# Performance work log

Hardware: AMD Instinct MI355X
Metric: run time of the kernel (lower is better)

The kernel has to match this reference:

```python
import jax, jax.numpy as jnp
import numpy as np

# Module hyperparameters (from init_kwargs / config defaults)
LOCAL_WINDOW = 128
GLOBAL_BUDGET = 64
ATT_BUDGET = 0.05
RANDOM_BUDGET = 0.1

B, S, D = 4, 4096, 1024


def setup_inputs() -> dict:
    key = jax.random.key(0)
    k1, k2 = jax.random.split(key)
    return {
        "hidden_states": jax.random.normal(k1, (B, S, D), dtype=jnp.float32),
        "attention_mask": jnp.ones((B, S), dtype=jnp.int32),
        "W_imp": jax.random.normal(k2, (1, D), dtype=jnp.float32) * 0.02,
    }


def _build_sparse_mask(hidden_states, attention_mask, W_imp):
    b, s, d = hidden_states.shape
    valid = attention_mask.astype(bool)                       # [b, s]
    # base mask: valid x valid, with causal constraint (is_decoder=True)
    i = jnp.arange(s)[:, None]
    j = jnp.arange(s)[None, :]
    causal = j <= i                                            # [s, s]
    base = (valid[:, None, :] & valid[:, :, None]) & causal[None]

    # 1) local causal sliding window: query i attends keys in [i-W+1, i]
    diff = i - j
    local = (diff >= 0) & (diff < LOCAL_WINDOW)                # [s, s]
    sparse = jnp.broadcast_to(local[None], (b, s, s))
    selected = jnp.broadcast_to(local.any(axis=0)[None], (b, s))

    # 2) global tokens via importance projection + top-k
    base_budget = min(GLOBAL_BUDGET, max(1, int(s * ATT_BUDGET)))
    scores = jnp.einsum('bsd,d->bs', hidden_states, W_imp[0])  # [b, s]
    scores = jnp.where(valid, scores, -jnp.inf)
    _, top_idx = jax.lax.top_k(scores, base_budget)            # [b, k]
    global_tokens = jnp.zeros((b, s), bool).at[
        jnp.arange(b)[:, None], top_idx].set(True)             # [b, s]
    # globals attend to everything and are attended by everything
    sparse = sparse | global_tokens[:, None, :] | global_tokens[:, :, None]
    selected = selected | global_tokens

    # 3) structured random tokens: deterministic strided selection
    r_budget = min(s, max(1, int(s * RANDOM_BUDGET)))
    stride = max(1, s // r_budget)
    rand_idx = (jnp.arange(r_budget) * stride) % s
    random_1d = jnp.zeros((s,), bool).at[rand_idx].set(True)
    random_tokens = jnp.broadcast_to(random_1d[None], (b, s))  # [b, s]
    sparse = sparse | random_tokens[:, None, :] | random_tokens[:, :, None]
    selected = selected | random_tokens

    # re-apply validity + causality
    sparse = sparse & base
    return sparse, selected, global_tokens, random_tokens


def reference(hidden_states, attention_mask, W_imp):
    b, s, _ = hidden_states.shape
    sparse, selected, gtok, rtok = _build_sparse_mask(
        hidden_states, attention_mask, W_imp)
    total_connections = sparse.sum(axis=(1, 2))
    attention_efficiency = total_connections.astype(jnp.float32) / float(s * s)
    # return sparse mask as float (the form consumed by attention), plus stats
    return (sparse.astype(jnp.float32), selected, attention_efficiency)
```

## Files before the change

### kernel.cpp

```cpp
#include <hip/hip_runtime.h>
#include <math.h>

#define BATCH 4
#define SEQ   4096
#define DIM   1024
#define TOPK  64
#define RSTRIDE 10
#define RBUDGET 409
#define LOCALW  128

typedef float nfloat4 __attribute__((ext_vector_type(4)));

#define WS_SCORES_OFF 0
#define WS_FLAGS_OFF  (BATCH * SEQ * sizeof(float))

__global__ void scores_kernel(const float* __restrict__ hs,
                              const int* __restrict__ amask,
                              const float* __restrict__ W,
                              float* __restrict__ scores) {
    int row  = blockIdx.x * 4 + (threadIdx.x >> 6);
    int lane = threadIdx.x & 63;
    const float4* h4 = (const float4*)(hs + (size_t)row * DIM);
    const float4* w4 = (const float4*)W;
    float acc = 0.0f;
#pragma unroll
    for (int k = 0; k < DIM / 4 / 64; ++k) {
        float4 h = h4[lane + 64 * k];
        float4 w = w4[lane + 64 * k];
        acc += h.x * w.x + h.y * w.y + h.z * w.z + h.w * w.w;
    }
#pragma unroll
    for (int off = 32; off; off >>= 1) acc += __shfl_down(acc, off, 64);
    if (lane == 0)
        scores[row] = amask[row] ? acc : -INFINITY;
}

__global__ void topk_flags_kernel(const float* __restrict__ scores,
                                  const int* __restrict__ amask,
                                  unsigned char* __restrict__ flags) {
    __shared__ unsigned int su[SEQ];
    __shared__ unsigned char gsel[SEQ];
    __shared__ unsigned int hist[257];
    __shared__ unsigned int sufA[257];
    __shared__ unsigned int sufB[257];
    __shared__ unsigned int bcast[2];

    int b = blockIdx.x, t = threadIdx.x;

    for (int k = t; k < SEQ; k += 256) {
        float s = scores[b * SEQ + k];
        unsigned int x = __float_as_uint(s);
        su[k] = (x & 0x80000000u) ? ~x : (x | 0x80000000u);
        gsel[k] = 0;
    }
    __syncthreads();

    unsigned int prefixVal = 0;
    unsigned int remaining = TOPK;
#pragma unroll
    for (int pass = 0; pass < 4; ++pass) {
        int shift = 24 - 8 * pass;
        unsigned int highmask = (pass == 0) ? 0u : (0xFFFFFFFFu << (shift + 8));

        hist[t] = 0;
        if (t == 0) hist[256] = 0;
        __syncthreads();

#pragma unroll
        for (int e = 0; e < SEQ / 256; ++e) {
            unsigned int u = su[t * (SEQ / 256) + e];
            if ((u & highmask) == prefixVal)
                atomicAdd(&hist[(u >> shift) & 0xFFu], 1u);
        }
        __syncthreads();

        sufA[t] = hist[t];
        if (t == 0) sufA[256] = 0;
        __syncthreads();
        unsigned int* src = sufA;
        unsigned int* dst = sufB;
        for (int d = 1; d < 256; d <<= 1) {
            unsigned int v = src[t] + ((t + d < 256) ? src[t + d] : 0u);
            dst[t] = v;
            if (t == 0) dst[256] = 0;
            __syncthreads();
            unsigned int* tmp = src; src = dst; dst = tmp;
        }
        if (src[t] >= remaining && src[t + 1] < remaining) {
            bcast[0] = (unsigned int)t;
            bcast[1] = remaining - src[t + 1];
        }
        __syncthreads();
        prefixVal |= (bcast[0] << shift);
        remaining = bcast[1];
        __syncthreads();
    }

    unsigned int T = prefixVal;
    unsigned int myeq = 0;
#pragma unroll
    for (int e = 0; e < SEQ / 256; ++e)
        if (su[t * (SEQ / 256) + e] == T) myeq++;
    sufA[t] = myeq;
    __syncthreads();
    {
        unsigned int* src = sufA;
        unsigned int* dst = sufB;
        for (int d = 1; d < 256; d <<= 1) {
            unsigned int v = src[t] + ((t >= d) ? src[t - d] : 0u);
            dst[t] = v;
            __syncthreads();
            unsigned int* tmp = src; src = dst; dst = tmp;
        }
        unsigned int taken = src[t] - myeq;
#pragma unroll
        for (int e = 0; e < SEQ / 256; ++e) {
            int idx = t * (SEQ / 256) + e;
            unsigned int u = su[idx];
            if (u > T) gsel[idx] = 1;
            else if (u == T) { if (taken < remaining) gsel[idx] = 1; taken++; }
        }
    }
    __syncthreads();

    for (int k = t; k < SEQ; k += 256) {
        int valid = (amask[b * SEQ + k] != 0) ? 1 : 0;
        int g = gsel[k];
        int r = ((k % RSTRIDE) == 0 && (k / RSTRIDE) < RBUDGET) ? 1 : 0;
        flags[b * SEQ + k] = (unsigned char)(valid | (g << 1) | (r << 2));
    }
}

__global__ void counts_kernel(const unsigned char* __restrict__ flags,
                              float* __restrict__ out_eff) {
    __shared__ int cumV[SEQ];
    __shared__ int cumH[SEQ];
    __shared__ int tvA[256], tvB[256], thA[256], thB[256];
    __shared__ int red[256];
    int b = blockIdx.x, t = threadIdx.x;
    int base = b * SEQ;

    int lv[16], lh[16];
    int sv = 0, sh = 0;
#pragma unroll
    for (int e = 0; e < 16; ++e) {
        unsigned char f = flags[base + t * 16 + e];
        int v = f & 1;
        int h = v & (((f & 6) != 0) ? 1 : 0);
        sv += v; sh += h;
        lv[e] = sv; lh[e] = sh;
    }
    tvA[t] = sv; thA[t] = sh;
    __syncthreads();
    int* vsrc = tvA; int* vdst = tvB;
    int* hsrc = thA; int* hdst = thB;
    for (int d = 1; d < 256; d <<= 1) {
        int av = vsrc[t] + ((t >= d) ? vsrc[t - d] : 0);
        int ah = hsrc[t] + ((t >= d) ? hsrc[t - d] : 0);
        vdst[t] = av; hdst[t] = ah;
        __syncthreads();
        int* tmp = vsrc; vsrc = vdst; vdst = tmp;
        tmp = hsrc; hsrc = hdst; hdst = tmp;
    }
    int bv = vsrc[t] - sv, bh = hsrc[t] - sh;
#pragma unroll
    for (int e = 0; e < 16; ++e) {
        cumV[t * 16 + e] = lv[e] + bv;
        cumH[t * 16 + e] = lh[e] + bh;
    }
    __syncthreads();

    int cnt = 0;
#pragma unroll
    for (int e = 0; e < 16; ++e) {
        int i = t * 16 + e;
        unsigned char f = flags[base + i];
        int validI = f & 1;
        int hotI = (f & 6) != 0;
        int c;
        if (hotI) c = cumV[i];
        else {
            int w = (i >= LOCALW) ? (cumV[i] - cumV[i - LOCALW]) : cumV[i];
            int g = (i >= LOCALW) ? cumH[i - LOCALW] : 0;
            c = w + g;
        }
        cnt += validI ? c : 0;
    }
    red[t] = cnt;
    __syncthreads();
    for (int s2 = 128; s2; s2 >>= 1) {
        if (t < s2) red[t] += red[t + s2];
        __syncthreads();
    }
    if (t == 0)
        out_eff[b] = (float)red[0] * (1.0f / ((float)SEQ * (float)SEQ));
}

__global__ void __launch_bounds__(256) mask_kernel(
        const unsigned char* __restrict__ flags,
        float* __restrict__ out) {
    int row0 = blockIdx.x << 2;
    int b = row0 >> 12;
    int t = threadIdx.x;

    const uchar4* f4 = (const uchar4*)(flags + b * SEQ);
    unsigned int validBits = 0, hotBits = 0;
#pragma unroll
    for (int k = 0; k < 4; ++k) {
        uchar4 f = f4[t + 256 * k];
        unsigned char fa[4] = {f.x, f.y, f.z, f.w};
#pragma unroll
        for (int e = 0; e < 4; ++e) {
            int idx = k * 4 + e;
            validBits |= (unsigned int)(fa[e] & 1u) << idx;
            hotBits   |= (unsigned int)((fa[e] & 6u) ? 1u : 0u) << idx;
        }
    }

    uchar4 fr = *(const uchar4*)(flags + row0);
    unsigned char fra[4] = {fr.x, fr.y, fr.z, fr.w};

#pragma unroll
    for (int r = 0; r < 4; ++r) {
        int i = (row0 + r) & (SEQ - 1);
        int validI = fra[r] & 1;
        int hotI = (fra[r] & 6) != 0;
        nfloat4* outrow4 = (nfloat4*)(out + (size_t)(row0 + r) * SEQ);
#pragma unroll
        for (int k = 0; k < 4; ++k) {
            int j4 = t + 256 * k;
            int j0 = j4 << 2;
            nfloat4 v;
#pragma unroll
            for (int e = 0; e < 4; ++e) {
                int idx = k * 4 + e;
                int j = j0 + e;
                int one = (j <= i) & validI & (int)((validBits >> idx) & 1u)
                        & (((i - j) < LOCALW) | hotI | (int)((hotBits >> idx) & 1u));
                v[e] = one ? 1.0f : 0.0f;
            }
            __builtin_nontemporal_store(v, outrow4 + j4);
        }
    }
}

__global__ void finalize_kernel(float* __restrict__ out_selected) {
    int idx = blockIdx.x * 256 + threadIdx.x;
    if (idx < BATCH * SEQ) out_selected[idx] = 1.0f;
}

extern "C" void kernel_launch(void* const* d_in, const int* in_sizes, int n_in,
                              void* d_out, int out_size, void* d_ws, size_t ws_size,
                              hipStream_t stream) {
    const float* hs    = (const float*)d_in[0];
    const int*   amask = (const int*)d_in[1];
    const float* W     = (const float*)d_in[2];

    char* ws = (char*)d_ws;
    float*         scores = (float*)(ws + WS_SCORES_OFF);
    unsigned char* flags  = (unsigned char*)(ws + WS_FLAGS_OFF);

    float* out_sparse   = (float*)d_out;
    float* out_selected = out_sparse + (size_t)BATCH * SEQ * SEQ;
    float* out_eff      = out_selected + BATCH * SEQ;

    scores_kernel<<<BATCH * SEQ / 4, 256, 0, stream>>>(hs, amask, W, scores);
    topk_flags_kernel<<<BATCH, 256, 0, stream>>>(scores, amask, flags);
    counts_kernel<<<BATCH, 256, 0, stream>>>(flags, out_eff);
    mask_kernel<<<BATCH * SEQ / 4, 256, 0, stream>>>(flags, out_sparse);
    finalize_kernel<<<(BATCH * SEQ + 255) / 256, 256, 0, stream>>>(out_selected);
}
```

Measured before the change: 336.3 us.

## Split mask writes into flag-independent and flag-dependent kernels, fuse topk/counts/finalize

The output mask is split into two regions. The part that depends only on the attention mask (causal window and the upper triangle) is written in the same launch as the top-k selection and the selected-ones fill. A second launch writes only the left region that depends on the global and random flags, and also computes the counts using bitmask popcounts instead of shared cumulative arrays. This cuts the launch count from five to three and overlaps the single-block top-k with the bulk store traffic. In exchange, the logic depends on the fixed window and column-boundary arithmetic, and the two kernels write disjoint pieces of the same output.

```diff
diff --git a/kernel.cpp b/kernel.cpp
--- a/kernel.cpp
+++ b/kernel.cpp
@@ -13,6 +13,11 @@
 
 #define WS_SCORES_OFF 0
 #define WS_FLAGS_OFF  (BATCH * SEQ * sizeof(float))
+
+#define X_TOPK_BLOCKS 4
+#define X_SEL_BLOCKS  16
+#define X_STATIC_BASE (X_TOPK_BLOCKS + X_SEL_BLOCKS)
+#define Y_CNT_BLOCKS  4
 
 __global__ void scores_kernel(const float* __restrict__ hs,
                               const int* __restrict__ amask,
@@ -35,9 +40,12 @@
         scores[row] = amask[row] ? acc : -INFINITY;
 }
 
-__global__ void topk_flags_kernel(const float* __restrict__ scores,
-                                  const int* __restrict__ amask,
-                                  unsigned char* __restrict__ flags) {
+__global__ void __launch_bounds__(256) fused_static_kernel(
+        const float* __restrict__ scores,
+        const int* __restrict__ amask,
+        unsigned char* __restrict__ flags,
+        float* __restrict__ out_sparse,
+        float* __restrict__ out_selected) {
     __shared__ unsigned int su[SEQ];
     __shared__ unsigned char gsel[SEQ];
     __shared__ unsigned int hist[257];
@@ -45,163 +53,219 @@
     __shared__ unsigned int sufB[257];
     __shared__ unsigned int bcast[2];
 
-    int b = blockIdx.x, t = threadIdx.x;
-
-    for (int k = t; k < SEQ; k += 256) {
-        float s = scores[b * SEQ + k];
-        unsigned int x = __float_as_uint(s);
-        su[k] = (x & 0x80000000u) ? ~x : (x | 0x80000000u);
-        gsel[k] = 0;
-    }
-    __syncthreads();
-
-    unsigned int prefixVal = 0;
-    unsigned int remaining = TOPK;
-#pragma unroll
-    for (int pass = 0; pass < 4; ++pass) {
-        int shift = 24 - 8 * pass;
-        unsigned int highmask = (pass == 0) ? 0u : (0xFFFFFFFFu << (shift + 8));
-
-        hist[t] = 0;
-        if (t == 0) hist[256] = 0;
-        __syncthreads();
-
-#pragma unroll
-        for (int e = 0; e < SEQ / 256; ++e) {
-            unsigned int u = su[t * (SEQ / 256) + e];
-            if ((u & highmask) == prefixVal)
-                atomicAdd(&hist[(u >> shift) & 0xFFu], 1u);
-        }
-        __syncthreads();
-
-        sufA[t] = hist[t];
-        if (t == 0) sufA[256] = 0;
-        __syncthreads();
-        unsigned int* src = sufA;
-        unsigned int* dst = sufB;
+    int bid = blockIdx.x;
+    int t = threadIdx.x;
+
+    if (bid < X_TOPK_BLOCKS) {
+        int b = bid;
+
+        for (int k = t; k < SEQ; k += 256) {
+            float s = scores[b * SEQ + k];
+            unsigned int x = __float_as_uint(s);
+            su[k] = (x & 0x80000000u) ? ~x : (x | 0x80000000u);
+            gsel[k] = 0;
+        }
+        __syncthreads();
+
+        unsigned int prefixVal = 0;
+        unsigned int remaining = TOPK;
+#pragma unroll
+        for (int pass = 0; pass < 4; ++pass) {
+            int shift = 24 - 8 * pass;
+            unsigned int highmask = (pass == 0) ? 0u : (0xFFFFFFFFu << (shift + 8));
+
+            hist[t] = 0;
+            if (t == 0) hist[256] = 0;
+            __syncthreads();
+
+#pragma unroll
+            for (int e = 0; e < SEQ / 256; ++e) {
+                unsigned int u = su[t * (SEQ / 256) + e];
+                if ((u & highmask) == prefixVal)
+                    atomicAdd(&hist[(u >> shift) & 0xFFu], 1u);
+            }
+            __syncthreads();
+
+            sufA[t] = hist[t];
+            if (t == 0) sufA[256] = 0;
+            __syncthreads();
+            unsigned int* src = sufA;
+            unsigned int* dst = sufB;
+            for (int d = 1; d < 256; d <<= 1) {
+                unsigned int v = src[t] + ((t + d < 256) ? src[t + d] : 0u);
+                dst[t] = v;
+                if (t == 0) dst[256] = 0;
+                __syncthreads();
+                unsigned int* tmp = src; src = dst; dst = tmp;
+            }
+            if (src[t] >= remaining && src[t + 1] < remaining) {
+                bcast[0] = (unsigned int)t;
+                bcast[1] = remaining - src[t + 1];
+            }
+            __syncthreads();
+            prefixVal |= (bcast[0] << shift);
+            remaining = bcast[1];
+            __syncthreads();
+        }
+
+        unsigned int T = prefixVal;
+        unsigned int myeq = 0;
+#pragma unroll
+        for (int e = 0; e < SEQ / 256; ++e)
+            if (su[t * (SEQ / 256) + e] == T) myeq++;
+        sufA[t] = myeq;
+        __syncthreads();
+        {
+            unsigned int* src = sufA;
+            unsigned int* dst = sufB;
+            for (int d = 1; d < 256; d <<= 1) {
+                unsigned int v = src[t] + ((t >= d) ? src[t - d] : 0u);
+                dst[t] = v;
+                __syncthreads();
+                unsigned int* tmp = src; src = dst; dst = tmp;
+            }
+            unsigned int taken = src[t] - myeq;
+#pragma unroll
+            for (int e = 0; e < SEQ / 256; ++e) {
+                int idx = t * (SEQ / 256) + e;
+                unsigned int u = su[idx];
+                if (u > T) gsel[idx] = 1;
+                else if (u == T) { if (taken < remaining) gsel[idx] = 1; taken++; }
+            }
+        }
+        __syncthreads();
+
+        for (int k = t; k < SEQ; k += 256) {
+            int valid = (amask[b * SEQ + k] != 0) ? 1 : 0;
+            int g = gsel[k];
+            int r = ((k % RSTRIDE) == 0 && (k / RSTRIDE) < RBUDGET) ? 1 : 0;
+            flags[b * SEQ + k] = (unsigned char)(valid | (g << 1) | (r << 2));
+        }
+        return;
+    }
+
+    if (bid < X_STATIC_BASE) {
+        int idx = (bid - X_TOPK_BLOCKS) * 256 + t;
+        nfloat4 ones = {1.0f, 1.0f, 1.0f, 1.0f};
+        __builtin_nontemporal_store(ones, ((nfloat4*)out_selected) + idx);
+        return;
+    }
+
+    int row0 = (bid - X_STATIC_BASE) << 2;
+    int b = row0 >> 12;
+
+    const int4* am4 = (const int4*)(amask + b * SEQ);
+    unsigned int validBits = 0;
+#pragma unroll
+    for (int k = 0; k < 4; ++k) {
+        int4 m = am4[t + 256 * k];
+        validBits |= (unsigned int)(m.x != 0) << (k * 4 + 0);
+        validBits |= (unsigned int)(m.y != 0) << (k * 4 + 1);
+        validBits |= (unsigned int)(m.z != 0) << (k * 4 + 2);
+        validBits |= (unsigned int)(m.w != 0) << (k * 4 + 3);
+    }
+    int4 mr = *(const int4*)(amask + row0);
+    int vIr[4] = {mr.x != 0, mr.y != 0, mr.z != 0, mr.w != 0};
+
+#pragma unroll
+    for (int r = 0; r < 4; ++r) {
+        int i = (row0 + r) & (SEQ - 1);
+        int vI = vIr[r];
+        int c4 = (i <= 127) ? 0 : (((i - 127 + 15) & ~15) >> 2);
+        nfloat4* outrow4 = (nfloat4*)(out_sparse + (size_t)(row0 + r) * SEQ);
+#pragma unroll
+        for (int k = 0; k < 4; ++k) {
+            int j4 = t + 256 * k;
+            if (j4 < c4) continue;
+            int j0 = j4 << 2;
+            nfloat4 v;
+#pragma unroll
+            for (int e = 0; e < 4; ++e) {
+                int j = j0 + e;
+                int one = (j <= i) & vI & (int)((validBits >> (k * 4 + e)) & 1u);
+                v[e] = one ? 1.0f : 0.0f;
+            }
+            __builtin_nontemporal_store(v, outrow4 + j4);
+        }
+    }
+}
+
+__global__ void __launch_bounds__(256) fused_dynamic_kernel(
+        const unsigned char* __restrict__ flags,
+        float* __restrict__ out_sparse,
+        float* __restrict__ out_eff) {
+    __shared__ unsigned int vb[256], hb[256];
+    __shared__ int tA[256], tB[256], tC[256], tD[256];
+    __shared__ int exV[256], exH[256];
+    __shared__ int red[256];
+
+    int bid = blockIdx.x, t = threadIdx.x;
+
+    if (bid < Y_CNT_BLOCKS) {
+        int b = bid, base = b * SEQ;
+        const unsigned char* fp = flags + base + t * 16;
+        unsigned int myv = 0, myh = 0;
+#pragma unroll
+        for (int e = 0; e < 16; ++e) {
+            unsigned char f = fp[e];
+            unsigned int v = f & 1u;
+            unsigned int h = v & ((f & 6u) ? 1u : 0u);
+            myv |= v << e;
+            myh |= h << e;
+        }
+        vb[t] = myv; hb[t] = myh;
+        int sv = __popc(myv), sh = __popc(myh);
+        tA[t] = sv; tC[t] = sh;
+        __syncthreads();
+        int* vsrc = tA; int* vdst = tB;
+        int* hsrc = tC; int* hdst = tD;
         for (int d = 1; d < 256; d <<= 1) {
-            unsigned int v = src[t] + ((t + d < 256) ? src[t + d] : 0u);
-            dst[t] = v;
-            if (t == 0) dst[256] = 0;
-            __syncthreads();
-            unsigned int* tmp = src; src = dst; dst = tmp;
-        }
-        if (src[t] >= remaining && src[t + 1] < remaining) {
-            bcast[0] = (unsigned int)t;
-            bcast[1] = remaining - src[t + 1];
-        }
-        __syncthreads();
-        prefixVal |= (bcast[0] << shift);
-        remaining = bcast[1];
-        __syncthreads();
-    }
-
-    unsigned int T = prefixVal;
-    unsigned int myeq = 0;
-#pragma unroll
-    for (int e = 0; e < SEQ / 256; ++e)
-        if (su[t * (SEQ / 256) + e] == T) myeq++;
-    sufA[t] = myeq;
-    __syncthreads();
-    {
-        unsigned int* src = sufA;
-        unsigned int* dst = sufB;
-        for (int d = 1; d < 256; d <<= 1) {
-            unsigned int v = src[t] + ((t >= d) ? src[t - d] : 0u);
-            dst[t] = v;
-            __syncthreads();
-            unsigned int* tmp = src; src = dst; dst = tmp;
-        }
-        unsigned int taken = src[t] - myeq;
-#pragma unroll
-        for (int e = 0; e < SEQ / 256; ++e) {
-            int idx = t * (SEQ / 256) + e;
-            unsigned int u = su[idx];
-            if (u > T) gsel[idx] = 1;
-            else if (u == T) { if (taken < remaining) gsel[idx] = 1; taken++; }
-        }
-    }
-    __syncthreads();
-
-    for (int k = t; k < SEQ; k += 256) {
-        int valid = (amask[b * SEQ + k] != 0) ? 1 : 0;
-        int g = gsel[k];
-        int r = ((k % RSTRIDE) == 0 && (k / RSTRIDE) < RBUDGET) ? 1 : 0;
-        flags[b * SEQ + k] = (unsigned char)(valid | (g << 1) | (r << 2));
-    }
-}
-
-__global__ void counts_kernel(const unsigned char* __restrict__ flags,
-                              float* __restrict__ out_eff) {
-    __shared__ int cumV[SEQ];
-    __shared__ int cumH[SEQ];
-    __shared__ int tvA[256], tvB[256], thA[256], thB[256];
-    __shared__ int red[256];
-    int b = blockIdx.x, t = threadIdx.x;
-    int base = b * SEQ;
-
-    int lv[16], lh[16];
-    int sv = 0, sh = 0;
-#pragma unroll
-    for (int e = 0; e < 16; ++e) {
-        unsigned char f = flags[base + t * 16 + e];
-        int v = f & 1;
-        int h = v & (((f & 6) != 0) ? 1 : 0);
-        sv += v; sh += h;
-        lv[e] = sv; lh[e] = sh;
-    }
-    tvA[t] = sv; thA[t] = sh;
-    __syncthreads();
-    int* vsrc = tvA; int* vdst = tvB;
-    int* hsrc = thA; int* hdst = thB;
-    for (int d = 1; d < 256; d <<= 1) {
-        int av = vsrc[t] + ((t >= d) ? vsrc[t - d] : 0);
-        int ah = hsrc[t] + ((t >= d) ? hsrc[t - d] : 0);
-        vdst[t] = av; hdst[t] = ah;
-        __syncthreads();
-        int* tmp = vsrc; vsrc = vdst; vdst = tmp;
-        tmp = hsrc; hsrc = hdst; hdst = tmp;
-    }
-    int bv = vsrc[t] - sv, bh = hsrc[t] - sh;
-#pragma unroll
-    for (int e = 0; e < 16; ++e) {
-        cumV[t * 16 + e] = lv[e] + bv;
-        cumH[t * 16 + e] = lh[e] + bh;
-    }
-    __syncthreads();
-
-    int cnt = 0;
-#pragma unroll
-    for (int e = 0; e < 16; ++e) {
-        int i = t * 16 + e;
-        unsigned char f = flags[base + i];
-        int validI = f & 1;
-        int hotI = (f & 6) != 0;
-        int c;
-        if (hotI) c = cumV[i];
-        else {
-            int w = (i >= LOCALW) ? (cumV[i] - cumV[i - LOCALW]) : cumV[i];
-            int g = (i >= LOCALW) ? cumH[i - LOCALW] : 0;
-            c = w + g;
-        }
-        cnt += validI ? c : 0;
-    }
-    red[t] = cnt;
-    __syncthreads();
-    for (int s2 = 128; s2; s2 >>= 1) {
-        if (t < s2) red[t] += red[t + s2];
-        __syncthreads();
-    }
-    if (t == 0)
-        out_eff[b] = (float)red[0] * (1.0f / ((float)SEQ * (float)SEQ));
-}
-
-__global__ void __launch_bounds__(256) mask_kernel(
-        const unsigned char* __restrict__ flags,
-        float* __restrict__ out) {
-    int row0 = blockIdx.x << 2;
+            int av = vsrc[t] + ((t >= d) ? vsrc[t - d] : 0);
+            int ah = hsrc[t] + ((t >= d) ? hsrc[t - d] : 0);
+            vdst[t] = av; hdst[t] = ah;
+            __syncthreads();
+            int* tmp = vsrc; vsrc = vdst; vdst = tmp;
+            tmp = hsrc; hsrc = hdst; hdst = tmp;
+        }
+        exV[t] = vsrc[t] - sv;
+        exH[t] = hsrc[t] - sh;
+        __syncthreads();
+
+        int exVt = exV[t];
+        int exV8 = (t >= 8) ? exV[t - 8] : 0;
+        int exH8 = (t >= 8) ? exH[t - 8] : 0;
+        unsigned int vb8 = (t >= 8) ? vb[t - 8] : 0u;
+        unsigned int hb8 = (t >= 8) ? hb[t - 8] : 0u;
+        int cnt = 0;
+#pragma unroll
+        for (int e = 0; e < 16; ++e) {
+            unsigned int m = (2u << e) - 1u;
+            int validI = (int)((myv >> e) & 1u);
+            int hotI   = (int)((myh >> e) & 1u);
+            int cumVi = exVt + __popc(myv & m);
+            int c;
+            if (t >= 8) {
+                int cumVm = exV8 + __popc(vb8 & m);
+                int cumHm = exH8 + __popc(hb8 & m);
+                c = hotI ? cumVi : (cumVi - cumVm + cumHm);
+            } else {
+                c = cumVi;
+            }
+            cnt += validI ? c : 0;
+        }
+        red[t] = cnt;
+        __syncthreads();
+        for (int s2 = 128; s2; s2 >>= 1) {
+            if (t < s2) red[t] += red[t + s2];
+            __syncthreads();
+        }
+        if (t == 0)
+            out_eff[b] = (float)red[0] * (1.0f / ((float)SEQ * (float)SEQ));
+        return;
+    }
+
+    int row0 = (bid - Y_CNT_BLOCKS) << 2;
     int b = row0 >> 12;
-    int t = threadIdx.x;
 
     const uchar4* f4 = (const uchar4*)(flags + b * SEQ);
     unsigned int validBits = 0, hotBits = 0;
@@ -216,37 +280,34 @@
             hotBits   |= (unsigned int)((fa[e] & 6u) ? 1u : 0u) << idx;
         }
     }
-
     uchar4 fr = *(const uchar4*)(flags + row0);
     unsigned char fra[4] = {fr.x, fr.y, fr.z, fr.w};
 
 #pragma unroll
     for (int r = 0; r < 4; ++r) {
         int i = (row0 + r) & (SEQ - 1);
-        int validI = fra[r] & 1;
+        if (i <= 127) continue;
+        int vI = fra[r] & 1;
         int hotI = (fra[r] & 6) != 0;
-        nfloat4* outrow4 = (nfloat4*)(out + (size_t)(row0 + r) * SEQ);
+        int c4 = ((i - 127 + 15) & ~15) >> 2;
+        nfloat4* outrow4 = (nfloat4*)(out_sparse + (size_t)(row0 + r) * SEQ);
 #pragma unroll
         for (int k = 0; k < 4; ++k) {
             int j4 = t + 256 * k;
+            if (j4 >= c4) continue;
             int j0 = j4 << 2;
             nfloat4 v;
 #pragma unroll
             for (int e = 0; e < 4; ++e) {
                 int idx = k * 4 + e;
                 int j = j0 + e;
-                int one = (j <= i) & validI & (int)((validBits >> idx) & 1u)
+                int one = vI & (int)((validBits >> idx) & 1u)
                         & (((i - j) < LOCALW) | hotI | (int)((hotBits >> idx) & 1u));
                 v[e] = one ? 1.0f : 0.0f;
             }
             __builtin_nontemporal_store(v, outrow4 + j4);
         }
     }
-}
-
-__global__ void finalize_kernel(float* __restrict__ out_selected) {
-    int idx = blockIdx.x * 256 + threadIdx.x;
-    if (idx < BATCH * SEQ) out_selected[idx] = 1.0f;
 }
 
 extern "C" void kernel_launch(void* const* d_in, const int* in_sizes, int n_in,
@@ -265,8 +326,8 @@
     float* out_eff      = out_selected + BATCH * SEQ;
 
     scores_kernel<<<BATCH * SEQ / 4, 256, 0, stream>>>(hs, amask, W, scores);
-    topk_flags_kernel<<<BATCH, 256, 0, stream>>>(scores, amask, flags);
-    counts_kernel<<<BATCH, 256, 0, stream>>>(flags, out_eff);
-    mask_kernel<<<BATCH * SEQ / 4, 256, 0, stream>>>(flags, out_sparse);
-    finalize_kernel<<<(BATCH * SEQ + 255) / 256, 256, 0, stream>>>(out_selected);
+    fused_static_kernel<<<X_STATIC_BASE + BATCH * SEQ / 4, 256, 0, stream>>>(
+        scores, amask, flags, out_sparse, out_selected);
+    fused_dynamic_kernel<<<Y_CNT_BLOCKS + BATCH * SEQ / 4, 256, 0, stream>>>(
+        flags, out_sparse, out_eff);
 }
```

Result: faster. 316.6 us (-5.9%).
